# Kernel tuning notes

Measured on AMD Instinct MI355X. Metric: run time of the kernel, lower is better.

## Reference

```python
import jax, jax.numpy as jnp
import numpy as np

NUM_LAYERS = 3
H_DIM = 2048
LN_EPS = 1e-5


def _linear(x, W, b):
    # 1x1x1 Conv3d == linear over the channel axis (last axis here)
    return jnp.einsum('...i,oi->...o', x, W) + b


def setup_inputs() -> dict:
    key = jax.random.key(0)
    ks = jax.random.split(key, 16)
    B, N, Cc, Cl, H = 64, 512, 2048, 2048, H_DIM
    s = 0.02
    inp = {
        'clip': jax.random.normal(ks[0], (B, Cc), jnp.float32),
        'lfb': jax.random.normal(ks[1], (B, N, Cl), jnp.float32),
        'Wc': jax.random.normal(ks[2], (H, Cc), jnp.float32) * s,
        'bc': jnp.zeros((H,), jnp.float32),
        'Wl': jax.random.normal(ks[3], (H, Cl), jnp.float32) * s,
        'bl': jnp.zeros((H,), jnp.float32),
        'Wt': jax.random.normal(ks[4], (H, H), jnp.float32) * s,
        'bt': jnp.zeros((H,), jnp.float32),
        'Wp': jax.random.normal(ks[5], (H, H), jnp.float32) * s,
        'bp': jnp.zeros((H,), jnp.float32),
        'Wg': jax.random.normal(ks[6], (H, H), jnp.float32) * s,
        'bg': jnp.zeros((H,), jnp.float32),
        'Wo': jax.random.normal(ks[7], (H, H), jnp.float32) * s,
        'bo': jnp.zeros((H,), jnp.float32),
    }
    return inp


def reference(clip, lfb, Wc, bc, Wl, bl, Wt, bt, Wp, bp, Wg, bg, Wo, bo):
    H = H_DIM
    scale = 1.0 / jnp.sqrt(jnp.asarray(H, clip.dtype))
    # process_clip / process_lfb (dropout = identity in eval)
    A = _linear(clip, Wc, bc)            # [B, H]
    Bfeat = _linear(lfb, Wl, bl)         # [B, N, H]
    # phi/g are layer-independent (shared weights, fixed Bfeat): hoist out of loop
    phi = _linear(Bfeat, Wp, bp)         # [B, N, H]
    g = _linear(Bfeat, Wg, bg)           # [B, N, H]
    out = A
    for _ in range(NUM_LAYERS):
        theta = _linear(A, Wt, bt)                                  # [B, H]
        scores = jnp.einsum('bh,bnh->bn', theta, phi) * scale       # [B, N]
        p = jax.nn.softmax(scores, axis=-1)                         # [B, N]
        t = jnp.einsum('bnh,bn->bh', g, p)                          # [B, H]
        # F.layer_norm over all non-batch dims (just H here), no affine
        mu = jnp.mean(t, axis=-1, keepdims=True)
        var = jnp.mean(jnp.square(t - mu), axis=-1, keepdims=True)
        ln = (t - mu) / jnp.sqrt(var + LN_EPS)
        h = _linear(jax.nn.relu(ln), Wo, bo)                        # [B, H]
        A = h + A
    out = A  # flattened view of [B, H, 1, 1, 1]
    loss = jnp.asarray(0.0, clip.dtype)  # nl_core returns (out, 0); loss is discarded
    return out, loss
```

## Files before the change

kernel.cpp:

```cpp
#include <hip/hip_runtime.h>

#define Bdim 64
#define Ndim 512
#define Hdim 2048
#define KSPLIT 8
#define NCHUNK 8
#define LNEPS 1e-5f
#define WMAT_ELEMS (Hdim * Hdim)

typedef unsigned short u16;
typedef __attribute__((ext_vector_type(8))) short short8;
typedef __attribute__((ext_vector_type(4))) float f32x4;

__device__ __forceinline__ u16 f2bf(float f) {
    unsigned int u = __float_as_uint(f);
    return (u16)((u + 0x7FFFu + ((u >> 16) & 1u)) >> 16);
}
__device__ __forceinline__ float bf2f(u16 s) {
    return __uint_as_float(((unsigned int)s) << 16);
}

__global__ __launch_bounds__(256)
void convert_w(const float* __restrict__ Wt, const float* __restrict__ Wl,
               const float* __restrict__ Wg, const float* __restrict__ Wo,
               const float* __restrict__ Wp, u16* __restrict__ dst)
{
    __shared__ float L[64][65];
    const int t   = threadIdx.x;
    const int bid = blockIdx.x;
    if (bid < 4096) {
        const int mid = bid >> 10;
        const int tb  = bid & 1023;
        const float* src = (mid == 0) ? Wt : (mid == 1) ? Wl : (mid == 2) ? Wg : Wo;
        u16* out = dst + (size_t)mid * WMAT_ELEMS;
        const size_t base = (size_t)tb * 4096 + (size_t)t * 16;
#pragma unroll
        for (int i = 0; i < 2; ++i) {
            float4 a = *(const float4*)(src + base + i * 8);
            float4 b = *(const float4*)(src + base + i * 8 + 4);
            short8 s;
            s[0] = (short)f2bf(a.x); s[1] = (short)f2bf(a.y);
            s[2] = (short)f2bf(a.z); s[3] = (short)f2bf(a.w);
            s[4] = (short)f2bf(b.x); s[5] = (short)f2bf(b.y);
            s[6] = (short)f2bf(b.z); s[7] = (short)f2bf(b.w);
            *(short8*)(out + base + i * 8) = s;
        }
    } else {
        const int mid = 4 + ((bid - 4096) >> 10);
        const int tb  = (bid - 4096) & 1023;
        const float* src = (mid == 4) ? Wp : Wl;
        u16* out = dst + (size_t)mid * WMAT_ELEMS;
        const int k0 = (tb & 31) * 64;
        const int o0 = (tb >> 5) * 64;
        const int row = t >> 2;
        const int cq  = t & 3;
#pragma unroll
        for (int i = 0; i < 4; ++i) {
            float4 v = *(const float4*)(src + (size_t)(k0 + row) * Hdim + o0 + cq * 16 + i * 4);
            *(float4*)(&L[row][cq * 16 + i * 4]) = v;
        }
        __syncthreads();
        const int orow = t >> 2;
#pragma unroll
        for (int half = 0; half < 2; ++half) {
            short8 s;
#pragma unroll
            for (int i = 0; i < 8; ++i)
                s[i] = (short)f2bf(L[cq * 16 + half * 8 + i][orow]);
            *(short8*)(out + (size_t)(o0 + orow) * Hdim + k0 + cq * 16 + half * 8) = s;
        }
    }
}

template<int XF32, int WF32>
__global__ __launch_bounds__(256)
void mfma_gemv(const u16* __restrict__ X16, const float* __restrict__ Xf,
               const u16* __restrict__ Wb, const float* __restrict__ Wf,
               float* __restrict__ part)
{
    __shared__ short Xs[64][72];
    __shared__ short Ws[64][72];
    const int t  = threadIdx.x;
    const int nt = blockIdx.x & 31;
    const int ks = blockIdx.x >> 5;
    const int o0 = nt * 64;
    const int kb = ks * 256;
    const int wv = t >> 6;
    const int ln = t & 63;
    const int xr = t & 63;
    const int xg = t >> 6;
    const int wn = t >> 2;
    const int wk = (t & 3) * 16;

    f32x4 acc[4];
#pragma unroll
    for (int i = 0; i < 4; ++i)
#pragma unroll
        for (int j = 0; j < 4; ++j) acc[i][j] = 0.f;

    uint4  qx[2];
    float4 px[4];
    uint4  qw[2];
    float4 pw[4];
    auto gload = [&](int k0) {
        if (!XF32) {
            qx[0] = *(const uint4*)(X16 + (size_t)xr * Hdim + k0 + xg * 16);
            qx[1] = *(const uint4*)(X16 + (size_t)xr * Hdim + k0 + xg * 16 + 8);
        } else {
#pragma unroll
            for (int i = 0; i < 4; ++i)
                px[i] = *(const float4*)(Xf + (size_t)xr * Hdim + k0 + xg * 16 + i * 4);
        }
        if (!WF32) {
            qw[0] = *(const uint4*)(Wb + (size_t)(o0 + wn) * Hdim + k0 + wk);
            qw[1] = *(const uint4*)(Wb + (size_t)(o0 + wn) * Hdim + k0 + wk + 8);
        } else {
#pragma unroll
            for (int i = 0; i < 4; ++i)
                pw[i] = *(const float4*)(Wf + (size_t)(o0 + wn) * Hdim + k0 + wk + i * 4);
        }
    };
    auto cvt8 = [](const float4& a, const float4& b) {
        short8 s;
        s[0] = (short)f2bf(a.x); s[1] = (short)f2bf(a.y);
        s[2] = (short)f2bf(a.z); s[3] = (short)f2bf(a.w);
        s[4] = (short)f2bf(b.x); s[5] = (short)f2bf(b.y);
        s[6] = (short)f2bf(b.z); s[7] = (short)f2bf(b.w);
        return s;
    };
    auto lstore = [&]() {
        if (!XF32) {
            *(uint4*)(&Xs[xr][xg * 16])     = qx[0];
            *(uint4*)(&Xs[xr][xg * 16 + 8]) = qx[1];
        } else {
            *(short8*)(&Xs[xr][xg * 16])     = cvt8(px[0], px[1]);
            *(short8*)(&Xs[xr][xg * 16 + 8]) = cvt8(px[2], px[3]);
        }
        if (!WF32) {
            *(uint4*)(&Ws[wn][wk])     = qw[0];
            *(uint4*)(&Ws[wn][wk + 8]) = qw[1];
        } else {
            *(short8*)(&Ws[wn][wk])     = cvt8(pw[0], pw[1]);
            *(short8*)(&Ws[wn][wk + 8]) = cvt8(pw[2], pw[3]);
        }
    };

    gload(kb);
    for (int c = 0; c < 4; ++c) {
        __syncthreads();
        lstore();
        __syncthreads();
        if (c < 3) gload(kb + (c + 1) * 64);
#pragma unroll
        for (int kstep = 0; kstep < 2; ++kstep) {
            const int kf = kstep * 32 + (ln >> 4) * 8;
            short8 af = *(const short8*)(&Xs[16 * wv + (ln & 15)][kf]);
#pragma unroll
            for (int n4 = 0; n4 < 4; ++n4) {
                short8 bf = *(const short8*)(&Ws[n4 * 16 + (ln & 15)][kf]);
                acc[n4] = __builtin_amdgcn_mfma_f32_16x16x32_bf16(af, bf, acc[n4], 0, 0, 0);
            }
        }
    }
#pragma unroll
    for (int n4 = 0; n4 < 4; ++n4) {
#pragma unroll
        for (int r = 0; r < 4; ++r) {
            const int brow = 16 * wv + (ln >> 4) * 4 + r;
            part[(size_t)(ks * 64 + brow) * Hdim + o0 + n4 * 16 + (ln & 15)] = acc[n4][r];
        }
    }
}

template<int HASBIAS, int ACC, int FINAL>
__global__ __launch_bounds__(256)
void combine(const float* __restrict__ part, const float* __restrict__ bias,
             float* __restrict__ Y, u16* __restrict__ Y16,
             float* __restrict__ out, int has_loss)
{
    const int flat4 = blockIdx.x * 256 + threadIdx.x;
    const size_t e  = (size_t)flat4 * 4;
    const int o     = (int)(e & (Hdim - 1));
    float4 v;
    if (HASBIAS) v = *(const float4*)(bias + o);
    else         v = make_float4(0.f, 0.f, 0.f, 0.f);
#pragma unroll
    for (int s = 0; s < KSPLIT; ++s) {
        float4 p = *(const float4*)(part + (size_t)s * (64 * Hdim) + e);
        v.x += p.x; v.y += p.y; v.z += p.z; v.w += p.w;
    }
    if (ACC) {
        float4 a = *(const float4*)(Y + e);
        v.x += a.x; v.y += a.y; v.z += a.z; v.w += a.w;
    }
    *(float4*)(Y + e) = v;
    ushort4 m;
    m.x = f2bf(v.x); m.y = f2bf(v.y); m.z = f2bf(v.z); m.w = f2bf(v.w);
    *(ushort4*)(Y16 + e) = m;
    if (FINAL) {
        *(float4*)(out + e) = v;
        if (has_loss && flat4 == 0) out[Bdim * Hdim] = 0.f;
    }
}

template<int FIRST>
__global__ __launch_bounds__(256, 4)
void flash_chunk(const float* __restrict__ lfb, const u16* __restrict__ lfb16r,
                 u16* __restrict__ lfb16w, const float* __restrict__ thpart,
                 float scale, u16* __restrict__ up,
                 float* __restrict__ wm, float* __restrict__ wz)
{
    __shared__ u16 T[NCHUNK][Hdim];
    __shared__ float th[Hdim];
    __shared__ float sc[NCHUNK];
    __shared__ float wts[NCHUNK];
    const int t  = threadIdx.x;
    const int b  = blockIdx.x >> 6;
    const int ch = blockIdx.x & 63;
    const size_t nbase = (size_t)b * Ndim + ch * NCHUNK;
#pragma unroll
    for (int i = 0; i < 16; ++i) {
        int flat4 = i * 256 + t;
        int row   = flat4 >> 9;
        int c4    = flat4 & 511;
        if (FIRST) {
            float4 v = *(const float4*)(lfb + (nbase + row) * Hdim + c4 * 4);
            ushort4 u4;
            u4.x = f2bf(v.x); u4.y = f2bf(v.y); u4.z = f2bf(v.z); u4.w = f2bf(v.w);
            *(ushort4*)(&T[row][c4 * 4]) = u4;
            *(ushort4*)(lfb16w + (nbase + row) * Hdim + c4 * 4) = u4;
        } else {
            ushort4 u4 = *(const ushort4*)(lfb16r + (nbase + row) * Hdim + c4 * 4);
            *(ushort4*)(&T[row][c4 * 4]) = u4;
        }
    }
#pragma unroll
    for (int i = 0; i < 2; ++i) {
        int c = (i * 256 + t) * 4;
        float4 v = make_float4(0.f, 0.f, 0.f, 0.f);
#pragma unroll
        for (int s = 0; s < KSPLIT; ++s) {
            float4 p = *(const float4*)(thpart + (size_t)(s * 64 + b) * Hdim + c);
            v.x += p.x; v.y += p.y; v.z += p.z; v.w += p.w;
        }
        *(float4*)(&th[c]) = v;
    }
    __syncthreads();
    const int wv = t >> 6, ln = t & 63;
#pragma unroll
    for (int q = 0; q < 2; ++q) {
        int n = wv * 2 + q;
        float a = 0.f;
#pragma unroll
        for (int i = 0; i < 8; ++i) {
            int c = ln * 4 + i * 256;
            ushort4 x = *(const ushort4*)(&T[n][c]);
            float4 y  = *(const float4*)(&th[c]);
            a += bf2f(x.x) * y.x + bf2f(x.y) * y.y + bf2f(x.z) * y.z + bf2f(x.w) * y.w;
        }
#pragma unroll
        for (int off = 32; off; off >>= 1) a += __shfl_xor(a, off, 64);
        if (ln == 0) sc[n] = a * scale;
    }
    __syncthreads();
    float m = sc[0];
#pragma unroll
    for (int n = 1; n < NCHUNK; ++n) m = fmaxf(m, sc[n]);
    if (t < NCHUNK) wts[t] = expf(sc[t] - m);
    __syncthreads();
    if (t == 0) {
        float z = 0.f;
#pragma unroll
        for (int n = 0; n < NCHUNK; ++n) z += wts[n];
        wm[blockIdx.x] = m;
        wz[blockIdx.x] = z;
    }
#pragma unroll
    for (int i = 0; i < 8; ++i) {
        int c = t + i * 256;
        float a = 0.f;
#pragma unroll
        for (int n = 0; n < NCHUNK; ++n) a += wts[n] * bf2f(T[n][c]);
        up[(size_t)blockIdx.x * Hdim + c] = f2bf(a);
    }
}

__global__ __launch_bounds__(256)
void flash_comb(const u16* __restrict__ up, const float* __restrict__ wm,
                const float* __restrict__ wz, u16* __restrict__ u16out)
{
    __shared__ float mm[64], zz[64], ee[64];
    const int t  = threadIdx.x;
    const int b  = blockIdx.x >> 3;
    const int sl = blockIdx.x & 7;
    if (t < 64) { mm[t] = wm[b * 64 + t]; zz[t] = wz[b * 64 + t]; }
    __syncthreads();
    float mg = mm[0];
#pragma unroll
    for (int i = 1; i < 64; ++i) mg = fmaxf(mg, mm[i]);
    if (t < 64) ee[t] = expf(mm[t] - mg);
    __syncthreads();
    float Z = 0.f;
#pragma unroll
    for (int i = 0; i < 64; ++i) Z += zz[i] * ee[i];
    const float inv = 1.f / Z;
    const int col = sl * 256 + t;
    float a = 0.f;
#pragma unroll 8
    for (int ch = 0; ch < 64; ++ch)
        a += ee[ch] * bf2f(up[(size_t)(b * 64 + ch) * Hdim + col]);
    u16out[(size_t)b * Hdim + col] = f2bf(a * inv);
}

__global__ __launch_bounds__(256)
void ln_relu_part(const float* __restrict__ part, const float* __restrict__ bias,
                  u16* __restrict__ r16)
{
    __shared__ float trow[Hdim];
    __shared__ float red[8];
    const int t = threadIdx.x, b = blockIdx.x;
    float sum = 0.f, sq = 0.f;
#pragma unroll
    for (int i = 0; i < 2; ++i) {
        int c = (i * 256 + t) * 4;
        float4 v = *(const float4*)(bias + c);
#pragma unroll
        for (int s = 0; s < KSPLIT; ++s) {
            float4 p = *(const float4*)(part + ((size_t)(s * 64 + b)) * Hdim + c);
            v.x += p.x; v.y += p.y; v.z += p.z; v.w += p.w;
        }
        *(float4*)(&trow[c]) = v;
        sum += v.x + v.y + v.z + v.w;
        sq  += v.x * v.x + v.y * v.y + v.z * v.z + v.w * v.w;
    }
#pragma unroll
    for (int off = 32; off; off >>= 1) {
        sum += __shfl_xor(sum, off, 64);
        sq  += __shfl_xor(sq,  off, 64);
    }
    if ((t & 63) == 0) { red[t >> 6] = sum; red[4 + (t >> 6)] = sq; }
    __syncthreads();
    sum = red[0] + red[1] + red[2] + red[3];
    sq  = red[4] + red[5] + red[6] + red[7];
    const float mu   = sum * (1.f / Hdim);
    const float var  = sq * (1.f / Hdim) - mu * mu;
    const float rstd = rsqrtf(var + LNEPS);
#pragma unroll
    for (int i = 0; i < 2; ++i) {
        int c = (i * 256 + t) * 4;
        float4 v = *(const float4*)(&trow[c]);
        ushort4 o;
        o.x = f2bf(fmaxf(0.f, (v.x - mu) * rstd));
        o.y = f2bf(fmaxf(0.f, (v.y - mu) * rstd));
        o.z = f2bf(fmaxf(0.f, (v.z - mu) * rstd));
        o.w = f2bf(fmaxf(0.f, (v.w - mu) * rstd));
        *(ushort4*)(r16 + (size_t)b * Hdim + c) = o;
    }
}

extern "C" void kernel_launch(void* const* d_in, const int* in_sizes, int n_in,
                              void* d_out, int out_size, void* d_ws, size_t ws_size,
                              hipStream_t stream) {
    (void)in_sizes; (void)n_in; (void)ws_size;
    const float* clip = (const float*)d_in[0];
    const float* lfb  = (const float*)d_in[1];
    const float* Wc   = (const float*)d_in[2];
    const float* bc   = (const float*)d_in[3];
    const float* Wl   = (const float*)d_in[4];
    const float* bl   = (const float*)d_in[5];
    const float* Wt   = (const float*)d_in[6];
    const float* bt   = (const float*)d_in[7];
    const float* Wp   = (const float*)d_in[8];
    const float* Wg   = (const float*)d_in[10];
    const float* bg   = (const float*)d_in[11];
    const float* Wo   = (const float*)d_in[12];
    const float* bo   = (const float*)d_in[13];
    float* out = (float*)d_out;

    float* wsf    = (float*)d_ws;
    float* A      = wsf;
    float* scrY   = wsf + 131072;
    u16*   A16    = (u16*)(wsf + 262144);
    u16*   th16   = (u16*)(wsf + 327680);
    u16*   tp16   = (u16*)(wsf + 393216);
    u16*   s16    = (u16*)(wsf + 458752);
    u16*   ubuf   = (u16*)(wsf + 524288);
    u16*   r16    = (u16*)(wsf + 589824);
    float* wm     = wsf + 655360;
    float* wz     = wsf + 659456;
    float* PA     = wsf + 663552;
    u16*   up     = (u16*)(wsf + 1712128);
    u16*   lfb16  = (u16*)(wsf + 5906432);
    u16*   Wbf    = (u16*)(wsf + 39460864);

    u16* bWt  = Wbf + (size_t)0 * WMAT_ELEMS;
    u16* bWl  = Wbf + (size_t)1 * WMAT_ELEMS;
    u16* bWg  = Wbf + (size_t)2 * WMAT_ELEMS;
    u16* bWo  = Wbf + (size_t)3 * WMAT_ELEMS;
    u16* bWpT = Wbf + (size_t)4 * WMAT_ELEMS;
    u16* bWlT = Wbf + (size_t)5 * WMAT_ELEMS;

    const float scale = 0.022097086912079608f;
    dim3 blk(256);
    const int has_loss = (out_size > Bdim * Hdim) ? 1 : 0;

    convert_w<<<6144, blk, 0, stream>>>(Wt, Wl, Wg, Wo, Wp, Wbf);

    mfma_gemv<1,1><<<256, blk, 0, stream>>>(nullptr, clip, nullptr, Wc, PA);
    combine<1,0,0><<<128, blk, 0, stream>>>(PA, bc, A, A16, nullptr, 0);

    for (int l = 0; l < 3; ++l) {
        mfma_gemv<0,0><<<256, blk, 0, stream>>>(A16, nullptr, bWt, nullptr, PA);
        combine<1,0,0><<<128, blk, 0, stream>>>(PA, bt, scrY, th16, nullptr, 0);
        mfma_gemv<0,0><<<256, blk, 0, stream>>>(th16, nullptr, bWpT, nullptr, PA);
        combine<0,0,0><<<128, blk, 0, stream>>>(PA, nullptr, scrY, tp16, nullptr, 0);
        mfma_gemv<0,0><<<256, blk, 0, stream>>>(tp16, nullptr, bWlT, nullptr, PA);
        if (l == 0)
            flash_chunk<1><<<4096, blk, 0, stream>>>(lfb, nullptr, lfb16, PA, scale, up, wm, wz);
        else
            flash_chunk<0><<<4096, blk, 0, stream>>>(nullptr, lfb16, nullptr, PA, scale, up, wm, wz);
        flash_comb<<<512, blk, 0, stream>>>(up, wm, wz, ubuf);
        mfma_gemv<0,0><<<256, blk, 0, stream>>>(ubuf, nullptr, bWl, nullptr, PA);
        combine<1,0,0><<<128, blk, 0, stream>>>(PA, bl, scrY, s16, nullptr, 0);
        mfma_gemv<0,0><<<256, blk, 0, stream>>>(s16, nullptr, bWg, nullptr, PA);
        ln_relu_part<<<64, blk, 0, stream>>>(PA, bg, r16);
        mfma_gemv<0,0><<<256, blk, 0, stream>>>(r16, nullptr, bWo, nullptr, PA);
        if (l < 2)
            combine<1,1,0><<<128, blk, 0, stream>>>(PA, bo, A, A16, nullptr, 0);
        else
            combine<1,1,1><<<128, blk, 0, stream>>>(PA, bo, A, A16, out, has_loss);
    }
}
```

Before: 427.1 us.

## Fuse small GEMV/combine chains into persistent kernels with grid barriers

Replaces the long sequence of small GEMV, combine, flash-combine and layernorm launches with persistent 256-block kernels that step through the stages, separated by atomic-counter grid barriers. Weight conversion is folded into the first persistent kernel. The theta split-K partials are reduced once into a separate buffer so flash_chunk reads the finished vector instead of summing eight partials. This removes many kernel launch gaps. The grid barrier assumes all 256 blocks are co-resident, which risks deadlock if they are not, and the barrier spin adds some overhead.

```diff
diff --git a/kernel.cpp b/kernel.cpp
--- a/kernel.cpp
+++ b/kernel.cpp
@@ -7,6 +7,7 @@
 #define NCHUNK 8
 #define LNEPS 1e-5f
 #define WMAT_ELEMS (Hdim * Hdim)
+#define GRIDP 256u
 
 typedef unsigned short u16;
 typedef __attribute__((ext_vector_type(8))) short short8;
@@ -20,17 +21,33 @@
     return __uint_as_float(((unsigned int)s) << 16);
 }
 
-__global__ __launch_bounds__(256)
-void convert_w(const float* __restrict__ Wt, const float* __restrict__ Wl,
-               const float* __restrict__ Wg, const float* __restrict__ Wo,
-               const float* __restrict__ Wp, u16* __restrict__ dst)
-{
-    __shared__ float L[64][65];
-    const int t   = threadIdx.x;
-    const int bid = blockIdx.x;
-    if (bid < 4096) {
-        const int mid = bid >> 10;
-        const int tb  = bid & 1023;
+__device__ __forceinline__ void gbar(unsigned* cnt) {
+    __syncthreads();
+    if (threadIdx.x == 0) {
+        __threadfence();
+        atomicAdd(cnt, 1u);
+        while (__hip_atomic_load(cnt, __ATOMIC_RELAXED, __HIP_MEMORY_SCOPE_AGENT) < GRIDP) {
+            __builtin_amdgcn_s_sleep(2);
+        }
+        __threadfence();
+    }
+    __syncthreads();
+}
+
+__global__ void init_k(unsigned* cnts) {
+    if (threadIdx.x < 64) cnts[threadIdx.x] = 0u;
+}
+
+
+__device__ void dev_convert(int v, const float* Wt, const float* Wl,
+                            const float* Wg, const float* Wo, const float* Wp,
+                            u16* dst, char* smRaw)
+{
+    float (*L)[65] = (float(*)[65])smRaw;
+    const int t = threadIdx.x;
+    if (v < 4096) {
+        const int mid = v >> 10;
+        const int tb  = v & 1023;
         const float* src = (mid == 0) ? Wt : (mid == 1) ? Wl : (mid == 2) ? Wg : Wo;
         u16* out = dst + (size_t)mid * WMAT_ELEMS;
         const size_t base = (size_t)tb * 4096 + (size_t)t * 16;
@@ -46,18 +63,19 @@
             *(short8*)(out + base + i * 8) = s;
         }
     } else {
-        const int mid = 4 + ((bid - 4096) >> 10);
-        const int tb  = (bid - 4096) & 1023;
+        const int mid = 4 + ((v - 4096) >> 10);
+        const int tb  = (v - 4096) & 1023;
         const float* src = (mid == 4) ? Wp : Wl;
         u16* out = dst + (size_t)mid * WMAT_ELEMS;
         const int k0 = (tb & 31) * 64;
         const int o0 = (tb >> 5) * 64;
         const int row = t >> 2;
         const int cq  = t & 3;
+        __syncthreads();
 #pragma unroll
         for (int i = 0; i < 4; ++i) {
-            float4 v = *(const float4*)(src + (size_t)(k0 + row) * Hdim + o0 + cq * 16 + i * 4);
-            *(float4*)(&L[row][cq * 16 + i * 4]) = v;
+            float4 v4 = *(const float4*)(src + (size_t)(k0 + row) * Hdim + o0 + cq * 16 + i * 4);
+            *(float4*)(&L[row][cq * 16 + i * 4]) = v4;
         }
         __syncthreads();
         const int orow = t >> 2;
@@ -73,13 +91,12 @@
 }
 
 template<int XF32, int WF32>
-__global__ __launch_bounds__(256)
-void mfma_gemv(const u16* __restrict__ X16, const float* __restrict__ Xf,
-               const u16* __restrict__ Wb, const float* __restrict__ Wf,
-               float* __restrict__ part)
-{
-    __shared__ short Xs[64][72];
-    __shared__ short Ws[64][72];
+__device__ void dev_gemv(const u16* X16, const float* Xf,
+                         const u16* Wb, const float* Wf,
+                         float* part, char* smRaw)
+{
+    short (*Xs)[72] = (short(*)[72])smRaw;
+    short (*Ws)[72] = (short(*)[72])(smRaw + 64 * 72 * 2);
     const int t  = threadIdx.x;
     const int nt = blockIdx.x & 31;
     const int ks = blockIdx.x >> 5;
@@ -173,12 +190,10 @@
 }
 
 template<int HASBIAS, int ACC, int FINAL>
-__global__ __launch_bounds__(256)
-void combine(const float* __restrict__ part, const float* __restrict__ bias,
-             float* __restrict__ Y, u16* __restrict__ Y16,
-             float* __restrict__ out, int has_loss)
-{
-    const int flat4 = blockIdx.x * 256 + threadIdx.x;
+__device__ void dev_combine(int bid, const float* part, const float* bias,
+                            float* Y, u16* Y16, float* out, int has_loss)
+{
+    const int flat4 = bid * 256 + threadIdx.x;
     const size_t e  = (size_t)flat4 * 4;
     const int o     = (int)(e & (Hdim - 1));
     float4 v;
@@ -203,10 +218,164 @@
     }
 }
 
+__device__ void dev_fcomb(int v, const u16* up, const float* wm,
+                          const float* wz, u16* u16out, char* smRaw)
+{
+    float* mm = (float*)smRaw;
+    float* zz = mm + 64;
+    float* ee = zz + 64;
+    const int t  = threadIdx.x;
+    const int b  = v >> 3;
+    const int sl = v & 7;
+    __syncthreads();
+    if (t < 64) { mm[t] = wm[b * 64 + t]; zz[t] = wz[b * 64 + t]; }
+    __syncthreads();
+    float mg = mm[0];
+#pragma unroll
+    for (int i = 1; i < 64; ++i) mg = fmaxf(mg, mm[i]);
+    if (t < 64) ee[t] = expf(mm[t] - mg);
+    __syncthreads();
+    float Z = 0.f;
+#pragma unroll
+    for (int i = 0; i < 64; ++i) Z += zz[i] * ee[i];
+    const float inv = 1.f / Z;
+    const int col = sl * 256 + t;
+    float a = 0.f;
+#pragma unroll 8
+    for (int ch = 0; ch < 64; ++ch)
+        a += ee[ch] * bf2f(up[(size_t)(b * 64 + ch) * Hdim + col]);
+    u16out[(size_t)b * Hdim + col] = f2bf(a * inv);
+}
+
+__device__ void dev_ln(int b, const float* part, const float* bias,
+                       u16* r16, char* smRaw)
+{
+    float* trow = (float*)smRaw;
+    float* red  = trow + Hdim;
+    const int t = threadIdx.x;
+    float sum = 0.f, sq = 0.f;
+#pragma unroll
+    for (int i = 0; i < 2; ++i) {
+        int c = (i * 256 + t) * 4;
+        float4 v = *(const float4*)(bias + c);
+#pragma unroll
+        for (int s = 0; s < KSPLIT; ++s) {
+            float4 p = *(const float4*)(part + ((size_t)(s * 64 + b)) * Hdim + c);
+            v.x += p.x; v.y += p.y; v.z += p.z; v.w += p.w;
+        }
+        *(float4*)(&trow[c]) = v;
+        sum += v.x + v.y + v.z + v.w;
+        sq  += v.x * v.x + v.y * v.y + v.z * v.z + v.w * v.w;
+    }
+#pragma unroll
+    for (int off = 32; off; off >>= 1) {
+        sum += __shfl_xor(sum, off, 64);
+        sq  += __shfl_xor(sq,  off, 64);
+    }
+    if ((t & 63) == 0) { red[t >> 6] = sum; red[4 + (t >> 6)] = sq; }
+    __syncthreads();
+    sum = red[0] + red[1] + red[2] + red[3];
+    sq  = red[4] + red[5] + red[6] + red[7];
+    const float mu   = sum * (1.f / Hdim);
+    const float var  = sq * (1.f / Hdim) - mu * mu;
+    const float rstd = rsqrtf(var + LNEPS);
+#pragma unroll
+    for (int i = 0; i < 2; ++i) {
+        int c = (i * 256 + t) * 4;
+        float4 v = *(const float4*)(&trow[c]);
+        ushort4 o;
+        o.x = f2bf(fmaxf(0.f, (v.x - mu) * rstd));
+        o.y = f2bf(fmaxf(0.f, (v.y - mu) * rstd));
+        o.z = f2bf(fmaxf(0.f, (v.z - mu) * rstd));
+        o.w = f2bf(fmaxf(0.f, (v.w - mu) * rstd));
+        *(ushort4*)(r16 + (size_t)b * Hdim + c) = o;
+    }
+}
+
+
+__global__ __launch_bounds__(256)
+void mega1(const float* clip, const float* Wc, const float* bc,
+           const float* Wt, const float* Wl, const float* Wg,
+           const float* Wo, const float* Wp, const float* bt,
+           u16* Wbf, float* PA, float* A, u16* A16, float* scrY,
+           u16* th16, u16* tp16, float* thetal, u16* junk16, unsigned* cnts)
+{
+    __shared__ char SM[18464];
+    const int bid = blockIdx.x;
+    u16* bWt  = Wbf;
+    u16* bWpT = Wbf + (size_t)4 * WMAT_ELEMS;
+    u16* bWlT = Wbf + (size_t)5 * WMAT_ELEMS;
+
+    for (int it = 0; it < 24; ++it)
+        dev_convert(it * 256 + bid, Wt, Wl, Wg, Wo, Wp, Wbf, SM);
+    dev_gemv<1,1>(nullptr, clip, nullptr, Wc, PA, SM);
+    gbar(cnts + 0);
+    if (bid < 128) dev_combine<1,0,0>(bid, PA, bc, A, A16, nullptr, 0);
+    gbar(cnts + 1);
+    dev_gemv<0,0>(A16, nullptr, bWt, nullptr, PA, SM);
+    gbar(cnts + 2);
+    if (bid < 128) dev_combine<1,0,0>(bid, PA, bt, scrY, th16, nullptr, 0);
+    gbar(cnts + 3);
+    dev_gemv<0,0>(th16, nullptr, bWpT, nullptr, PA, SM);
+    gbar(cnts + 4);
+    if (bid < 128) dev_combine<0,0,0>(bid, PA, nullptr, scrY, tp16, nullptr, 0);
+    gbar(cnts + 5);
+    dev_gemv<0,0>(tp16, nullptr, bWlT, nullptr, PA, SM);
+    gbar(cnts + 6);
+    if (bid < 128) dev_combine<0,0,0>(bid, PA, nullptr, thetal, junk16, nullptr, 0);
+}
+
+template<int NEXT, int FINAL>
+__global__ __launch_bounds__(256)
+void mega2(const u16* up, const float* wm, const float* wz, u16* ubuf,
+           u16* Wbf, float* PA, const float* bl, float* scrY, u16* s16,
+           const float* bg, u16* r16, const float* bo, float* A, u16* A16,
+           float* out, int has_loss, const float* bt,
+           u16* th16, u16* tp16, float* thetal, u16* junk16, unsigned* cnts)
+{
+    __shared__ char SM[18464];
+    const int bid = blockIdx.x;
+    u16* bWt  = Wbf;
+    u16* bWl  = Wbf + (size_t)1 * WMAT_ELEMS;
+    u16* bWg  = Wbf + (size_t)2 * WMAT_ELEMS;
+    u16* bWo  = Wbf + (size_t)3 * WMAT_ELEMS;
+    u16* bWpT = Wbf + (size_t)4 * WMAT_ELEMS;
+    u16* bWlT = Wbf + (size_t)5 * WMAT_ELEMS;
+
+    dev_fcomb(bid * 2 + 0, up, wm, wz, ubuf, SM);
+    dev_fcomb(bid * 2 + 1, up, wm, wz, ubuf, SM);
+    gbar(cnts + 0);
+    dev_gemv<0,0>(ubuf, nullptr, bWl, nullptr, PA, SM);
+    gbar(cnts + 1);
+    if (bid < 128) dev_combine<1,0,0>(bid, PA, bl, scrY, s16, nullptr, 0);
+    gbar(cnts + 2);
+    dev_gemv<0,0>(s16, nullptr, bWg, nullptr, PA, SM);
+    gbar(cnts + 3);
+    if (bid < 64) dev_ln(bid, PA, bg, r16, SM);
+    gbar(cnts + 4);
+    dev_gemv<0,0>(r16, nullptr, bWo, nullptr, PA, SM);
+    gbar(cnts + 5);
+    if (bid < 128) dev_combine<1,1,FINAL>(bid, PA, bo, A, A16, out, has_loss);
+    if (NEXT) {
+        gbar(cnts + 6);
+        dev_gemv<0,0>(A16, nullptr, bWt, nullptr, PA, SM);
+        gbar(cnts + 7);
+        if (bid < 128) dev_combine<1,0,0>(bid, PA, bt, scrY, th16, nullptr, 0);
+        gbar(cnts + 8);
+        dev_gemv<0,0>(th16, nullptr, bWpT, nullptr, PA, SM);
+        gbar(cnts + 9);
+        if (bid < 128) dev_combine<0,0,0>(bid, PA, nullptr, scrY, tp16, nullptr, 0);
+        gbar(cnts + 10);
+        dev_gemv<0,0>(tp16, nullptr, bWlT, nullptr, PA, SM);
+        gbar(cnts + 11);
+        if (bid < 128) dev_combine<0,0,0>(bid, PA, nullptr, thetal, junk16, nullptr, 0);
+    }
+}
+
 template<int FIRST>
 __global__ __launch_bounds__(256, 4)
 void flash_chunk(const float* __restrict__ lfb, const u16* __restrict__ lfb16r,
-                 u16* __restrict__ lfb16w, const float* __restrict__ thpart,
+                 u16* __restrict__ lfb16w, const float* __restrict__ thetal,
                  float scale, u16* __restrict__ up,
                  float* __restrict__ wm, float* __restrict__ wz)
 {
@@ -237,12 +406,7 @@
 #pragma unroll
     for (int i = 0; i < 2; ++i) {
         int c = (i * 256 + t) * 4;
-        float4 v = make_float4(0.f, 0.f, 0.f, 0.f);
-#pragma unroll
-        for (int s = 0; s < KSPLIT; ++s) {
-            float4 p = *(const float4*)(thpart + (size_t)(s * 64 + b) * Hdim + c);
-            v.x += p.x; v.y += p.y; v.z += p.z; v.w += p.w;
-        }
+        float4 v = *(const float4*)(thetal + (size_t)b * Hdim + c);
         *(float4*)(&th[c]) = v;
     }
     __syncthreads();
@@ -282,79 +446,6 @@
 #pragma unroll
         for (int n = 0; n < NCHUNK; ++n) a += wts[n] * bf2f(T[n][c]);
         up[(size_t)blockIdx.x * Hdim + c] = f2bf(a);
-    }
-}
-
-__global__ __launch_bounds__(256)
-void flash_comb(const u16* __restrict__ up, const float* __restrict__ wm,
-                const float* __restrict__ wz, u16* __restrict__ u16out)
-{
-    __shared__ float mm[64], zz[64], ee[64];
-    const int t  = threadIdx.x;
-    const int b  = blockIdx.x >> 3;
-    const int sl = blockIdx.x & 7;
-    if (t < 64) { mm[t] = wm[b * 64 + t]; zz[t] = wz[b * 64 + t]; }
-    __syncthreads();
-    float mg = mm[0];
-#pragma unroll
-    for (int i = 1; i < 64; ++i) mg = fmaxf(mg, mm[i]);
-    if (t < 64) ee[t] = expf(mm[t] - mg);
-    __syncthreads();
-    float Z = 0.f;
-#pragma unroll
-    for (int i = 0; i < 64; ++i) Z += zz[i] * ee[i];
-    const float inv = 1.f / Z;
-    const int col = sl * 256 + t;
-    float a = 0.f;
-#pragma unroll 8
-    for (int ch = 0; ch < 64; ++ch)
-        a += ee[ch] * bf2f(up[(size_t)(b * 64 + ch) * Hdim + col]);
-    u16out[(size_t)b * Hdim + col] = f2bf(a * inv);
-}
-
-__global__ __launch_bounds__(256)
-void ln_relu_part(const float* __restrict__ part, const float* __restrict__ bias,
-                  u16* __restrict__ r16)
-{
-    __shared__ float trow[Hdim];
-    __shared__ float red[8];
-    const int t = threadIdx.x, b = blockIdx.x;
-    float sum = 0.f, sq = 0.f;
-#pragma unroll
-    for (int i = 0; i < 2; ++i) {
-        int c = (i * 256 + t) * 4;
-        float4 v = *(const float4*)(bias + c);
-#pragma unroll
-        for (int s = 0; s < KSPLIT; ++s) {
-            float4 p = *(const float4*)(part + ((size_t)(s * 64 + b)) * Hdim + c);
-            v.x += p.x; v.y += p.y; v.z += p.z; v.w += p.w;
-        }
-        *(float4*)(&trow[c]) = v;
-        sum += v.x + v.y + v.z + v.w;
-        sq  += v.x * v.x + v.y * v.y + v.z * v.z + v.w * v.w;
-    }
-#pragma unroll
-    for (int off = 32; off; off >>= 1) {
-        sum += __shfl_xor(sum, off, 64);
-        sq  += __shfl_xor(sq,  off, 64);
-    }
-    if ((t & 63) == 0) { red[t >> 6] = sum; red[4 + (t >> 6)] = sq; }
-    __syncthreads();
-    sum = red[0] + red[1] + red[2] + red[3];
-    sq  = red[4] + red[5] + red[6] + red[7];
-    const float mu   = sum * (1.f / Hdim);
-    const float var  = sq * (1.f / Hdim) - mu * mu;
-    const float rstd = rsqrtf(var + LNEPS);
-#pragma unroll
-    for (int i = 0; i < 2; ++i) {
-        int c = (i * 256 + t) * 4;
-        float4 v = *(const float4*)(&trow[c]);
-        ushort4 o;
-        o.x = f2bf(fmaxf(0.f, (v.x - mu) * rstd));
-        o.y = f2bf(fmaxf(0.f, (v.y - mu) * rstd));
-        o.z = f2bf(fmaxf(0.f, (v.z - mu) * rstd));
-        o.w = f2bf(fmaxf(0.f, (v.w - mu) * rstd));
-        *(ushort4*)(r16 + (size_t)b * Hdim + c) = o;
     }
 }
 
@@ -377,57 +468,43 @@
     const float* bo   = (const float*)d_in[13];
     float* out = (float*)d_out;
 
-    float* wsf    = (float*)d_ws;
-    float* A      = wsf;
-    float* scrY   = wsf + 131072;
-    u16*   A16    = (u16*)(wsf + 262144);
-    u16*   th16   = (u16*)(wsf + 327680);
-    u16*   tp16   = (u16*)(wsf + 393216);
-    u16*   s16    = (u16*)(wsf + 458752);
-    u16*   ubuf   = (u16*)(wsf + 524288);
-    u16*   r16    = (u16*)(wsf + 589824);
-    float* wm     = wsf + 655360;
-    float* wz     = wsf + 659456;
-    float* PA     = wsf + 663552;
-    u16*   up     = (u16*)(wsf + 1712128);
-    u16*   lfb16  = (u16*)(wsf + 5906432);
-    u16*   Wbf    = (u16*)(wsf + 39460864);
-
-    u16* bWt  = Wbf + (size_t)0 * WMAT_ELEMS;
-    u16* bWl  = Wbf + (size_t)1 * WMAT_ELEMS;
-    u16* bWg  = Wbf + (size_t)2 * WMAT_ELEMS;
-    u16* bWo  = Wbf + (size_t)3 * WMAT_ELEMS;
-    u16* bWpT = Wbf + (size_t)4 * WMAT_ELEMS;
-    u16* bWlT = Wbf + (size_t)5 * WMAT_ELEMS;
+    float*    wsf    = (float*)d_ws;
+    float*    A      = wsf;
+    float*    scrY   = wsf + 131072;
+    float*    thetal = wsf + 262144;
+    u16*      A16    = (u16*)(wsf + 393216);
+    u16*      th16   = (u16*)(wsf + 458752);
+    u16*      tp16   = (u16*)(wsf + 524288);
+    u16*      s16    = (u16*)(wsf + 589824);
+    u16*      ubuf   = (u16*)(wsf + 655360);
+    u16*      r16    = (u16*)(wsf + 720896);
+    u16*      junk16 = (u16*)(wsf + 786432);
+    float*    wm     = wsf + 851968;
+    float*    wz     = wsf + 856064;
+    unsigned* cnts   = (unsigned*)(wsf + 860160);
+    float*    PA     = wsf + 860224;
+    u16*      up     = (u16*)(wsf + 1908800);
+    u16*      lfb16  = (u16*)(wsf + 6103104);
+    u16*      Wbf    = (u16*)(wsf + 39657536);
 
     const float scale = 0.022097086912079608f;
+    const int has_loss = (out_size > Bdim * Hdim) ? 1 : 0;
     dim3 blk(256);
-    const int has_loss = (out_size > Bdim * Hdim) ? 1 : 0;
-
-    convert_w<<<6144, blk, 0, stream>>>(Wt, Wl, Wg, Wo, Wp, Wbf);
-
-    mfma_gemv<1,1><<<256, blk, 0, stream>>>(nullptr, clip, nullptr, Wc, PA);
-    combine<1,0,0><<<128, blk, 0, stream>>>(PA, bc, A, A16, nullptr, 0);
-
-    for (int l = 0; l < 3; ++l) {
-        mfma_gemv<0,0><<<256, blk, 0, stream>>>(A16, nullptr, bWt, nullptr, PA);
-        combine<1,0,0><<<128, blk, 0, stream>>>(PA, bt, scrY, th16, nullptr, 0);
-        mfma_gemv<0,0><<<256, blk, 0, stream>>>(th16, nullptr, bWpT, nullptr, PA);
-        combine<0,0,0><<<128, blk, 0, stream>>>(PA, nullptr, scrY, tp16, nullptr, 0);
-        mfma_gemv<0,0><<<256, blk, 0, stream>>>(tp16, nullptr, bWlT, nullptr, PA);
-        if (l == 0)
-            flash_chunk<1><<<4096, blk, 0, stream>>>(lfb, nullptr, lfb16, PA, scale, up, wm, wz);
-        else
-            flash_chunk<0><<<4096, blk, 0, stream>>>(nullptr, lfb16, nullptr, PA, scale, up, wm, wz);
-        flash_comb<<<512, blk, 0, stream>>>(up, wm, wz, ubuf);
-        mfma_gemv<0,0><<<256, blk, 0, stream>>>(ubuf, nullptr, bWl, nullptr, PA);
-        combine<1,0,0><<<128, blk, 0, stream>>>(PA, bl, scrY, s16, nullptr, 0);
-        mfma_gemv<0,0><<<256, blk, 0, stream>>>(s16, nullptr, bWg, nullptr, PA);
-        ln_relu_part<<<64, blk, 0, stream>>>(PA, bg, r16);
-        mfma_gemv<0,0><<<256, blk, 0, stream>>>(r16, nullptr, bWo, nullptr, PA);
-        if (l < 2)
-            combine<1,1,0><<<128, blk, 0, stream>>>(PA, bo, A, A16, nullptr, 0);
-        else
-            combine<1,1,1><<<128, blk, 0, stream>>>(PA, bo, A, A16, out, has_loss);
-    }
-}
+
+    init_k<<<1, 64, 0, stream>>>(cnts);
+    mega1<<<256, blk, 0, stream>>>(clip, Wc, bc, Wt, Wl, Wg, Wo, Wp, bt,
+                                   Wbf, PA, A, A16, scrY, th16, tp16, thetal,
+                                   junk16, cnts + 0);
+    flash_chunk<1><<<4096, blk, 0, stream>>>(lfb, nullptr, lfb16, thetal, scale, up, wm, wz);
+    mega2<1,0><<<256, blk, 0, stream>>>(up, wm, wz, ubuf, Wbf, PA, bl, scrY, s16,
+                                        bg, r16, bo, A, A16, nullptr, 0, bt,
+                                        th16, tp16, thetal, junk16, cnts + 7);
+    flash_chunk<0><<<4096, blk, 0, stream>>>(nullptr, lfb16, nullptr, thetal, scale, up, wm, wz);
+    mega2<1,0><<<256, blk, 0, stream>>>(up, wm, wz, ubuf, Wbf, PA, bl, scrY, s16,
+                                        bg, r16, bo, A, A16, nullptr, 0, bt,
+                                        th16, tp16, thetal, junk16, cnts + 19);
+    flash_chunk<0><<<4096, blk, 0, stream>>>(nullptr, lfb16, nullptr, thetal, scale, up, wm, wz);
+    mega2<0,1><<<256, blk, 0, stream>>>(up, wm, wz, ubuf, Wbf, PA, bl, scrY, s16,
+                                        bg, r16, bo, A, A16, out, has_loss, bt,
+                                        th16, tp16, thetal, junk16, cnts + 31);
+}
```

Measured after the change: 1.269 ms. 197% more time.
